# Performance work log

Measured on AMD Instinct MI355X. Metric: run time of the kernel, lower is better.

The kernel has to match this reference:

```python
import jax, jax.numpy as jnp
import numpy as np

DICT_SIZE = 16384
D_MODEL = 1024
TOP_K = 8
B, T = 2, 2048


def setup_inputs() -> dict:
    key = jax.random.key(0)
    k1, k2, k3 = jax.random.split(key, 3)
    x = jax.random.normal(k1, (B, T, D_MODEL), dtype=jnp.float32)
    # nn.Linear weight, scaled small like the torch init style
    W_enc = jax.random.normal(k2, (DICT_SIZE, D_MODEL), dtype=jnp.float32) * 0.02
    # unified dictionary: randn * 0.02 per UnifiedDictionaryCore
    W_dict = jax.random.normal(k3, (DICT_SIZE, D_MODEL), dtype=jnp.float32) * 0.02
    return {"x": x, "W_enc": W_enc, "W_dict": W_dict}


def reference(x, W_enc, W_dict):
    # encoder: Linear(d_model -> dict_size), no bias
    coeffs = jnp.einsum("btd,md->btm", x, W_enc)  # [B,T,dict_size]
    topk_vals, topk_idx = jax.lax.top_k(coeffs, TOP_K)  # [B,T,K]
    # scatter-into-zeros then dense matmul == weighted sum of gathered dict rows
    # (top-k indices are unique per token, so the math is identical)
    rows = W_dict[topk_idx]  # [B,T,K,d_model]
    offset = jnp.einsum("btk,btkd->btd", topk_vals, rows)
    # sparse_coeffs.abs().mean() over the full dense [B,T,dict_size] tensor;
    # only the top-k entries are nonzero
    sparsity_loss = jnp.sum(jnp.abs(topk_vals)) / (coeffs.size)
    return offset, sparsity_loss
```

## Files before the change

kernel.cpp:

```cpp
#include <hip/hip_runtime.h>
#include <float.h>
#include <stdint.h>

constexpr int D_MODEL = 1024;
constexpr int DICT    = 16384;
constexpr int TOPK    = 8;
constexpr int NCAND   = 16;
constexpr int NTOK    = 4096;
constexpr int NTILE   = 128;
constexpr long long COEFF_COUNT = (long long)NTOK * DICT;

typedef __attribute__((ext_vector_type(8))) __bf16 bf16x8;
typedef __attribute__((ext_vector_type(4))) float  floatx4;

__device__ __forceinline__ unsigned short f2bf(float f) {
    unsigned int u = __float_as_uint(f);
    u = u + 0x7fffu + ((u >> 16) & 1u);
    return (unsigned short)(u >> 16);
}

__device__ __forceinline__ void async16(void* lds, const void* g) {
    __builtin_amdgcn_global_load_lds(
        (__attribute__((address_space(1))) void*)g,
        (__attribute__((address_space(3))) void*)lds, 16, 0, 0);
}

__global__ __launch_bounds__(256) void ssod_cvt2(const float4* __restrict__ xs, ushort4* __restrict__ xd, int nx4,
                                                 const float4* __restrict__ ws, ushort4* __restrict__ wd, int nw4) {
    const int i = blockIdx.x * 256 + threadIdx.x;
    if (i < nx4) {
        const float4 v = xs[i];
        ushort4 o; o.x = f2bf(v.x); o.y = f2bf(v.y); o.z = f2bf(v.z); o.w = f2bf(v.w);
        xd[i] = o;
    } else {
        const int j = i - nx4;
        if (j < nw4) {
            const float4 v = ws[j];
            ushort4 o; o.x = f2bf(v.x); o.y = f2bf(v.y); o.z = f2bf(v.z); o.w = f2bf(v.w);
            wd[j] = o;
        }
    }
}

__global__ __launch_bounds__(256) void ssod_gemm_bf16(const unsigned short* __restrict__ A,
                                                      const unsigned short* __restrict__ B,
                                                      unsigned short* __restrict__ C,
                                                      unsigned short* __restrict__ tmax) {
    __shared__ unsigned short As[128 * 32];
    __shared__ unsigned short Bs[128 * 32];
    __shared__ unsigned int rmax[128];

    const int tid  = threadIdx.x;
    const int wave = tid >> 6;
    const int lane = tid & 63;
    const int bn   = blockIdx.x;
    const int bm   = blockIdx.y;
    const int wm   = wave >> 1;
    const int wn   = wave & 1;

    const unsigned short* Abase = A + (size_t)bm * 128 * D_MODEL;
    const unsigned short* Bbase = B + (size_t)bn * 128 * D_MODEL;

    floatx4 acc[4][4];
    #pragma unroll
    for (int i = 0; i < 4; ++i)
        #pragma unroll
        for (int j = 0; j < 4; ++j) acc[i][j] = floatx4{0.f, 0.f, 0.f, 0.f};

    const int c0 = wave * 64 + lane;
    const int c1 = c0 + 256;

    const int fr = lane & 15;
    const int kg = lane >> 4;

    for (int k0 = 0; k0 < D_MODEL; k0 += 32) {
        async16(&As[c0 * 8], Abase + (size_t)(c0 >> 2) * D_MODEL + k0 + (c0 & 3) * 8);
        async16(&As[c1 * 8], Abase + (size_t)(c1 >> 2) * D_MODEL + k0 + (c1 & 3) * 8);
        async16(&Bs[c0 * 8], Bbase + (size_t)(c0 >> 2) * D_MODEL + k0 + (c0 & 3) * 8);
        async16(&Bs[c1 * 8], Bbase + (size_t)(c1 >> 2) * D_MODEL + k0 + (c1 & 3) * 8);
        __syncthreads();

        bf16x8 af[4], bfr[4];
        #pragma unroll
        for (int f = 0; f < 4; ++f) {
            af[f]  = *(const bf16x8*)&As[(wm * 64 + f * 16 + fr) * 32 + kg * 8];
            bfr[f] = *(const bf16x8*)&Bs[(wn * 64 + f * 16 + fr) * 32 + kg * 8];
        }
        #pragma unroll
        for (int i = 0; i < 4; ++i)
            #pragma unroll
            for (int j = 0; j < 4; ++j)
                acc[i][j] = __builtin_amdgcn_mfma_f32_16x16x32_bf16(af[i], bfr[j], acc[i][j], 0, 0, 0);
        __syncthreads();
    }

    if (tid < 128) rmax[tid] = 0;

    const int col = lane & 15;
    const int rq  = lane >> 4;
    unsigned int rowm[4][4];
    #pragma unroll
    for (int i = 0; i < 4; ++i)
        #pragma unroll
        for (int r = 0; r < 4; ++r) rowm[i][r] = 0;

    #pragma unroll
    for (int i = 0; i < 4; ++i) {
        const int row = bm * 128 + wm * 64 + i * 16 + rq * 4;
        #pragma unroll
        for (int j = 0; j < 4; ++j) {
            const int ccol = bn * 128 + wn * 64 + j * 16 + col;
            unsigned short* cp = C + (size_t)row * DICT + ccol;
            #pragma unroll
            for (int r = 0; r < 4; ++r) {
                const unsigned short bf = f2bf(acc[i][j][r]);
                cp[(size_t)r * DICT] = bf;
                rowm[i][r] = max(rowm[i][r], (unsigned int)(bf ^ 0x8000u));
            }
        }
    }
    __syncthreads();

    #pragma unroll
    for (int i = 0; i < 4; ++i)
        #pragma unroll
        for (int r = 0; r < 4; ++r) {
            unsigned int m = rowm[i][r];
            m = max(m, (unsigned int)__shfl_xor((int)m, 1, 64));
            m = max(m, (unsigned int)__shfl_xor((int)m, 2, 64));
            m = max(m, (unsigned int)__shfl_xor((int)m, 4, 64));
            m = max(m, (unsigned int)__shfl_xor((int)m, 8, 64));
            if ((lane & 15) == 0)
                atomicMax(&rmax[wm * 64 + i * 16 + rq * 4 + r], m);
        }
    __syncthreads();

    if (tid < 128)
        tmax[(size_t)(bm * 128 + tid) * NTILE + bn] = (unsigned short)rmax[tid];
}

__device__ __forceinline__ bool tk_better(float v1, int i1, float v2, int i2) {
    return (v1 > v2) || (v1 == v2 && i1 < i2);
}

__global__ __launch_bounds__(256) void ssod_select_refine(const unsigned short* __restrict__ coeffs,
                                                          const unsigned short* __restrict__ tmax,
                                                          const float* __restrict__ x,
                                                          const float* __restrict__ Wenc,
                                                          const float* __restrict__ Wdict,
                                                          float* __restrict__ outp,
                                                          float* __restrict__ tsum,
                                                          int tokBase) {
    const int tl   = blockIdx.x;
    const int t    = tokBase + tl;
    const int tid  = threadIdx.x;
    const int lane = tid & 63;
    const int wave = tid >> 6;

    __shared__ unsigned int keys[128];
    __shared__ int   tlist[64];
    __shared__ int   ncnt, kcnt;
    __shared__ unsigned int sTau;
    __shared__ float xs[D_MODEL];
    __shared__ int   cidx[NCAND];
    __shared__ float cval[NCAND];
    __shared__ float sval[TOPK];
    __shared__ int   sidx[TOPK];

    ((float4*)xs)[tid] = ((const float4*)(x + (size_t)t * D_MODEL))[tid];
    if (tid == 0) { ncnt = 0; kcnt = 0; }
    __syncthreads();

    const unsigned short* tmrow = tmax + (size_t)t * NTILE;
    if (wave == 0) {
        const unsigned int u = ((const unsigned int*)tmrow)[lane];
        unsigned int v0 = u & 0xFFFFu, v1 = u >> 16;
        for (int k = 2; k <= 128; k <<= 1) {
            for (int j = k >> 1; j >= 1; j >>= 1) {
                if (j == 64) {
                    const unsigned int a = max(v0, v1), b = min(v0, v1);
                    v0 = a; v1 = b;
                } else {
                    const unsigned int p0 = __shfl_xor(v0, j, 64);
                    const unsigned int p1 = __shfl_xor(v1, j, 64);
                    const bool tm0 = ((lane & j) == 0) ^ ((( lane      ) & k) != 0);
                    const bool tm1 = ((lane & j) == 0) ^ (((lane + 64) & k) != 0);
                    v0 = tm0 ? max(v0, p0) : min(v0, p0);
                    v1 = tm1 ? max(v1, p1) : min(v1, p1);
                }
            }
        }
        if (lane == 15) sTau = v0;
    }
    __syncthreads();
    const unsigned int tau = sTau;

    if (tid < NTILE) {
        if ((unsigned int)tmrow[tid] >= tau) {
            const int p = atomicAdd(&ncnt, 1);
            if (p < 64) tlist[p] = tid;
        }
    }
    __syncthreads();
    const int nq = min(ncnt, 64);

    const uint4* row4 = (const uint4*)(coeffs + (size_t)tl * DICT);
    for (int j = tid; j < nq * 16; j += 256) {
        const int tile = tlist[j >> 4];
        const int sub  = j & 15;
        const uint4 p = row4[tile * 16 + sub];
        unsigned int w[4] = {p.x ^ 0x80008000u, p.y ^ 0x80008000u,
                             p.z ^ 0x80008000u, p.w ^ 0x80008000u};
        const int base = tile * 128 + sub * 8;
        #pragma unroll
        for (int h = 0; h < 4; ++h) {
            const unsigned int lo = w[h] & 0xFFFFu, hi = w[h] >> 16;
            if (lo >= tau) {
                const int q = atomicAdd(&kcnt, 1);
                if (q < 128) keys[q] = (lo << 16) | (unsigned)(16383 - (base + h * 2));
            }
            if (hi >= tau) {
                const int q = atomicAdd(&kcnt, 1);
                if (q < 128) keys[q] = (hi << 16) | (unsigned)(16383 - (base + h * 2 + 1));
            }
        }
    }
    __syncthreads();
    const int m = min(kcnt, 128);
    for (int i = m + tid; i < 128; i += 256) keys[i] = 0;
    __syncthreads();

    if (wave == 0) {
        unsigned int v0 = keys[lane], v1 = keys[lane + 64];
        for (int k = 2; k <= 128; k <<= 1) {
            for (int j = k >> 1; j >= 1; j >>= 1) {
                if (j == 64) {
                    const unsigned int a = max(v0, v1), b = min(v0, v1);
                    v0 = a; v1 = b;
                } else {
                    const unsigned int p0 = __shfl_xor(v0, j, 64);
                    const unsigned int p1 = __shfl_xor(v1, j, 64);
                    const bool tm0 = ((lane & j) == 0) ^ ((( lane      ) & k) != 0);
                    const bool tm1 = ((lane & j) == 0) ^ (((lane + 64) & k) != 0);
                    v0 = tm0 ? max(v0, p0) : min(v0, p0);
                    v1 = tm1 ? max(v1, p1) : min(v1, p1);
                }
            }
        }
        if (lane < NCAND) cidx[lane] = 16383 - (int)(v0 & 0xFFFFu);
    }
    __syncthreads();

    const float4* xs4 = (const float4*)xs;
    float4 xv[4];
    #pragma unroll
    for (int q = 0; q < 4; ++q) xv[q] = xs4[q * 64 + lane];

    float4 wv[4][4];
    #pragma unroll
    for (int s = 0; s < 4; ++s) {
        const float4* wr4 = (const float4*)(Wenc + (size_t)cidx[s * 4 + wave] * D_MODEL);
        #pragma unroll
        for (int q = 0; q < 4; ++q) wv[s][q] = wr4[q * 64 + lane];
    }
    #pragma unroll
    for (int s = 0; s < 4; ++s) {
        float sum = 0.f;
        #pragma unroll
        for (int q = 0; q < 4; ++q)
            sum += xv[q].x * wv[s][q].x + xv[q].y * wv[s][q].y +
                   xv[q].z * wv[s][q].z + xv[q].w * wv[s][q].w;
        #pragma unroll
        for (int off = 32; off > 0; off >>= 1) sum += __shfl_down(sum, off, 64);
        if (lane == 0) cval[s * 4 + wave] = sum;
    }
    __syncthreads();

    if (tid < NCAND) {
        const float v = cval[tid];
        const int  ix = cidx[tid];
        int rank = 0;
        #pragma unroll
        for (int j = 0; j < NCAND; ++j)
            rank += (j != tid) && tk_better(cval[j], cidx[j], v, ix);
        if (rank < TOPK) { sval[rank] = v; sidx[rank] = ix; }
    }
    __syncthreads();
    if (tid == 0) {
        float s = 0.f;
        #pragma unroll
        for (int k = 0; k < TOPK; ++k) s += fabsf(sval[k]);
        tsum[t] = s;
    }

    const int dd = tid * 4;
    float4 a = make_float4(0.f, 0.f, 0.f, 0.f);
    #pragma unroll
    for (int k = 0; k < TOPK; ++k) {
        const float4 r = *(const float4*)(Wdict + (size_t)sidx[k] * D_MODEL + dd);
        const float s = sval[k];
        a.x += s * r.x; a.y += s * r.y; a.z += s * r.z; a.w += s * r.w;
    }
    *(float4*)(outp + (size_t)t * D_MODEL + dd) = a;
}

__global__ __launch_bounds__(256) void ssod_loss(const float* __restrict__ tsum,
                                                 float* __restrict__ out) {
    float s = 0.f;
    for (int i = threadIdx.x; i < NTOK; i += 256) s += tsum[i];
    #pragma unroll
    for (int off = 32; off > 0; off >>= 1) s += __shfl_down(s, off, 64);
    __shared__ float wsum[4];
    if ((threadIdx.x & 63) == 0) wsum[threadIdx.x >> 6] = s;
    __syncthreads();
    if (threadIdx.x == 0) {
        const float tot = wsum[0] + wsum[1] + wsum[2] + wsum[3];
        out[(size_t)NTOK * D_MODEL] = tot / (float)COEFF_COUNT;
    }
}

extern "C" void kernel_launch(void* const* d_in, const int* in_sizes, int n_in,
                              void* d_out, int out_size, void* d_ws, size_t ws_size,
                              hipStream_t stream) {
    const float* x     = (const float*)d_in[0];
    const float* Wenc  = (const float*)d_in[1];
    const float* Wdict = (const float*)d_in[2];
    float* out = (float*)d_out;

    char* ws = (char*)d_ws;
    size_t off = 0;
    unsigned short* xbf  = (unsigned short*)(ws + off); off += (size_t)NTOK * D_MODEL * 2;
    unsigned short* wbf  = (unsigned short*)(ws + off); off += (size_t)DICT * D_MODEL * 2;
    unsigned short* tmax = (unsigned short*)(ws + off); off += (size_t)NTOK * NTILE * 2;
    float* tsum = (float*)(ws + off);                   off += (size_t)NTOK * 4;
    unsigned short* coeffs = (unsigned short*)(ws + off);

    const size_t remain = (ws_size > off) ? (ws_size - off) : 0;
    int chunk = 512;
    if (remain >= (size_t)4096 * DICT * 2) chunk = 4096;
    else if (remain >= (size_t)2048 * DICT * 2) chunk = 2048;
    else if (remain >= (size_t)1024 * DICT * 2) chunk = 1024;

    const int nx4 = NTOK * D_MODEL / 4;
    const int nw4 = DICT * D_MODEL / 4;
    ssod_cvt2<<<(nx4 + nw4 + 255) / 256, 256, 0, stream>>>(
        (const float4*)x, (ushort4*)xbf, nx4, (const float4*)Wenc, (ushort4*)wbf, nw4);

    for (int tokBase = 0; tokBase < NTOK; tokBase += chunk) {
        dim3 g(DICT / 128, chunk / 128);
        ssod_gemm_bf16<<<g, 256, 0, stream>>>(xbf + (size_t)tokBase * D_MODEL, wbf, coeffs,
                                              tmax + (size_t)tokBase * NTILE);
        ssod_select_refine<<<chunk, 256, 0, stream>>>(coeffs, tmax, x, Wenc, Wdict, out, tsum, tokBase);
    }
    ssod_loss<<<1, 256, 0, stream>>>(tsum, out);
}
```

Before: 393.6 us.

## Rewrite encoder GEMM with 256x256 tiles, 4-stage async pipeline and swizzled LDS

Replaces the 128x128 single-buffered bf16 GEMM with a 512-thread, 256x256-tile kernel. It uses a 4-deep ring of LDS buffers filled by async global-to-LDS loads, XOR-swizzled LDS layout to avoid bank conflicts, interleaved barriers with s_setprio around MFMA bursts, and an XCD-aware block remapping. This targets load latency exposure and low arithmetic intensity in the old GEMM, at the cost of higher register and LDS pressure. The kernel now hardcodes 32 k-tiles and requires the chunk size to be a multiple of 256.

```diff
diff --git a/kernel.cpp b/kernel.cpp
--- a/kernel.cpp
+++ b/kernel.cpp
@@ -42,102 +42,165 @@
     }
 }
 
-__global__ __launch_bounds__(256) void ssod_gemm_bf16(const unsigned short* __restrict__ A,
-                                                      const unsigned short* __restrict__ B,
-                                                      unsigned short* __restrict__ C,
-                                                      unsigned short* __restrict__ tmax) {
-    __shared__ unsigned short As[128 * 32];
-    __shared__ unsigned short Bs[128 * 32];
-    __shared__ unsigned int rmax[128];
+constexpr size_t R1OFF = (size_t)128 * (D_MODEL * 2);
+
+#define STAGE_A(buf_, t_) do {                                               \
+    const char* s_ = pA + (size_t)(t_) * 64;                                 \
+    char* d_ = (char*)&As[(buf_)][0] + wave * 1024;                          \
+    async16(d_, s_); async16(d_ + 8192, s_ + R1OFF);                         \
+} while (0)
+
+#define STAGE_B(buf_, t_) do {                                               \
+    const char* s_ = pB + (size_t)(t_) * 64;                                 \
+    char* d_ = (char*)&Bs[(buf_)][0] + wave * 1024;                          \
+    async16(d_, s_); async16(d_ + 8192, s_ + R1OFF);                         \
+} while (0)
+
+#define MFMA4(a_, r_)                                                                        \
+    acc[r_][0] = __builtin_amdgcn_mfma_f32_16x16x32_bf16(a_, bq0, acc[r_][0], 0, 0, 0);      \
+    acc[r_][1] = __builtin_amdgcn_mfma_f32_16x16x32_bf16(a_, bq1, acc[r_][1], 0, 0, 0);      \
+    acc[r_][2] = __builtin_amdgcn_mfma_f32_16x16x32_bf16(a_, bq2, acc[r_][2], 0, 0, 0);      \
+    acc[r_][3] = __builtin_amdgcn_mfma_f32_16x16x32_bf16(a_, bq3, acc[r_][3], 0, 0, 0);
+
+#define TILE_BODY(T_, DOSTAGE_)                                              \
+  {                                                                          \
+    const int buf_ = (T_) & 3;                                               \
+    const char* ab_ = (const char*)As + buf_ * 16384 + aob;                  \
+    const char* bb_ = (const char*)Bs + buf_ * 16384 + bob;                  \
+    bf16x8 af0 = *(const bf16x8*)(ab_);                                      \
+    bf16x8 af1 = *(const bf16x8*)(ab_ + 1024);                               \
+    bf16x8 af2 = *(const bf16x8*)(ab_ + 2048);                               \
+    bf16x8 af3 = *(const bf16x8*)(ab_ + 3072);                               \
+    bf16x8 bq0 = *(const bf16x8*)(bb_);                                      \
+    bf16x8 bq1 = *(const bf16x8*)(bb_ + 1024);                               \
+    bf16x8 bq2 = *(const bf16x8*)(bb_ + 2048);                               \
+    bf16x8 bq3 = *(const bf16x8*)(bb_ + 3072);                               \
+    if (DOSTAGE_) { STAGE_A(((T_) + 3) & 3, (T_) + 3); }                     \
+    __builtin_amdgcn_s_barrier();                                            \
+    asm volatile("s_waitcnt lgkmcnt(0)" ::: "memory");                       \
+    __builtin_amdgcn_s_setprio(1);                                           \
+    MFMA4(af0, 0); MFMA4(af1, 1); MFMA4(af2, 2); MFMA4(af3, 3);              \
+    __builtin_amdgcn_s_setprio(0);                                           \
+    __builtin_amdgcn_s_barrier();                                            \
+    bf16x8 ag0 = *(const bf16x8*)(ab_ + 4096);                               \
+    bf16x8 ag1 = *(const bf16x8*)(ab_ + 5120);                               \
+    bf16x8 ag2 = *(const bf16x8*)(ab_ + 6144);                               \
+    bf16x8 ag3 = *(const bf16x8*)(ab_ + 7168);                               \
+    if (DOSTAGE_) { STAGE_B(((T_) + 3) & 3, (T_) + 3); }                     \
+    __builtin_amdgcn_s_barrier();                                            \
+    asm volatile("s_waitcnt lgkmcnt(0)" ::: "memory");                       \
+    __builtin_amdgcn_s_setprio(1);                                           \
+    MFMA4(ag0, 4); MFMA4(ag1, 5); MFMA4(ag2, 6); MFMA4(ag3, 7);              \
+    __builtin_amdgcn_s_setprio(0);                                           \
+  }
+
+#define TILE_CLOSE(VMI)                                                      \
+    asm volatile("s_waitcnt vmcnt(" #VMI ")" ::: "memory");                  \
+    __builtin_amdgcn_s_barrier();
+
+__global__ __launch_bounds__(512, 2) void ssod_gemm_bf16(const unsigned short* __restrict__ A,
+                                                         const unsigned short* __restrict__ B,
+                                                         unsigned short* __restrict__ C,
+                                                         unsigned short* __restrict__ tmax,
+                                                         int mtiles) {
+    __shared__ __align__(16) unsigned short As[4][8192];
+    __shared__ __align__(16) unsigned short Bs[4][8192];
 
     const int tid  = threadIdx.x;
     const int wave = tid >> 6;
     const int lane = tid & 63;
-    const int bn   = blockIdx.x;
-    const int bm   = blockIdx.y;
-    const int wm   = wave >> 1;
-    const int wn   = wave & 1;
-
-    const unsigned short* Abase = A + (size_t)bm * 128 * D_MODEL;
-    const unsigned short* Bbase = B + (size_t)bn * 128 * D_MODEL;
-
-    floatx4 acc[4][4];
-    #pragma unroll
-    for (int i = 0; i < 4; ++i)
-        #pragma unroll
-        for (int j = 0; j < 4; ++j) acc[i][j] = floatx4{0.f, 0.f, 0.f, 0.f};
-
-    const int c0 = wave * 64 + lane;
-    const int c1 = c0 + 256;
-
+
+    const int nwg = mtiles * 64;
+    const int cpx = nwg >> 3;
+    const int bid = blockIdx.x;
+    const int vid = (bid & 7) * cpx + (bid >> 3);
+    const int bn  = vid & 63;
+    const int bm  = vid >> 6;
+
+    const int wm = wave >> 2;
+    const int wn = wave & 3;
     const int fr = lane & 15;
     const int kg = lane >> 4;
 
-    for (int k0 = 0; k0 < D_MODEL; k0 += 32) {
-        async16(&As[c0 * 8], Abase + (size_t)(c0 >> 2) * D_MODEL + k0 + (c0 & 3) * 8);
-        async16(&As[c1 * 8], Abase + (size_t)(c1 >> 2) * D_MODEL + k0 + (c1 & 3) * 8);
-        async16(&Bs[c0 * 8], Bbase + (size_t)(c0 >> 2) * D_MODEL + k0 + (c0 & 3) * 8);
-        async16(&Bs[c1 * 8], Bbase + (size_t)(c1 >> 2) * D_MODEL + k0 + (c1 & 3) * 8);
-        __syncthreads();
-
-        bf16x8 af[4], bfr[4];
-        #pragma unroll
-        for (int f = 0; f < 4; ++f) {
-            af[f]  = *(const bf16x8*)&As[(wm * 64 + f * 16 + fr) * 32 + kg * 8];
-            bfr[f] = *(const bf16x8*)&Bs[(wn * 64 + f * 16 + fr) * 32 + kg * 8];
-        }
-        #pragma unroll
-        for (int i = 0; i < 4; ++i)
-            #pragma unroll
-            for (int j = 0; j < 4; ++j)
-                acc[i][j] = __builtin_amdgcn_mfma_f32_16x16x32_bf16(af[i], bfr[j], acc[i][j], 0, 0, 0);
-        __syncthreads();
-    }
-
-    if (tid < 128) rmax[tid] = 0;
-
-    const int col = lane & 15;
-    const int rq  = lane >> 4;
-    unsigned int rowm[4][4];
-    #pragma unroll
-    for (int i = 0; i < 4; ++i)
-        #pragma unroll
-        for (int r = 0; r < 4; ++r) rowm[i][r] = 0;
-
-    #pragma unroll
-    for (int i = 0; i < 4; ++i) {
-        const int row = bm * 128 + wm * 64 + i * 16 + rq * 4;
-        #pragma unroll
-        for (int j = 0; j < 4; ++j) {
-            const int ccol = bn * 128 + wn * 64 + j * 16 + col;
-            unsigned short* cp = C + (size_t)row * DICT + ccol;
+    const int sR   = tid >> 3;
+    const int sinp = ((tid & 7) * 16) ^ ((sR & 7) << 4);
+    const int smr  = 2 * sR + (sinp >> 6);
+    const int skb  = sinp & 63;
+    const char* pA = (const char*)(A + (size_t)bm * 256 * D_MODEL) + (size_t)smr * (D_MODEL * 2) + skb;
+    const char* pB = (const char*)(B + (size_t)bn * 256 * D_MODEL) + (size_t)smr * (D_MODEL * 2) + skb;
+
+    const int swz = ((((fr & 1) << 6) | (kg << 4)) ^ (((fr >> 1) & 7) << 4));
+    const int aob = (wm * 64 + (fr >> 1)) * 128 + swz;
+    const int bob = (wn * 32 + (fr >> 1)) * 128 + swz;
+
+    floatx4 acc[8][4];
+    #pragma unroll
+    for (int i = 0; i < 8; ++i)
+        #pragma unroll
+        for (int j = 0; j < 4; ++j) acc[i][j] = floatx4{0.f, 0.f, 0.f, 0.f};
+
+    STAGE_A(0, 0); STAGE_B(0, 0);
+    STAGE_A(1, 1); STAGE_B(1, 1);
+    STAGE_A(2, 2); STAGE_B(2, 2);
+    TILE_CLOSE(8)
+
+    #pragma unroll 1
+    for (int T = 0; T < 29; ++T) {
+        TILE_BODY(T, true)
+        TILE_CLOSE(8)
+    }
+    TILE_BODY(29, false)
+    TILE_CLOSE(4)
+    TILE_BODY(30, false)
+    TILE_CLOSE(0)
+    TILE_BODY(31, false)
+
+    __syncthreads();
+    unsigned int* rmax = (unsigned int*)&As[0][0];
+    rmax[tid] = 0;
+    __syncthreads();
+
+    const int col  = lane & 15;
+    const int rq   = lane >> 4;
+    const int half = wn >> 1;
+    const size_t colbase = (size_t)bn * 256 + wn * 64 + col;
+
+    #pragma unroll
+    for (int mf = 0; mf < 8; ++mf) {
+        const int rowl = wm * 128 + mf * 16 + rq * 4;
+        unsigned int rm[4] = {0, 0, 0, 0};
+        #pragma unroll
+        for (int nf = 0; nf < 4; ++nf) {
+            unsigned short* cp = C + (size_t)(bm * 256 + rowl) * DICT + colbase + nf * 16;
             #pragma unroll
             for (int r = 0; r < 4; ++r) {
-                const unsigned short bf = f2bf(acc[i][j][r]);
-                cp[(size_t)r * DICT] = bf;
-                rowm[i][r] = max(rowm[i][r], (unsigned int)(bf ^ 0x8000u));
+                const unsigned short bfv = f2bf(acc[mf][nf][r]);
+                cp[(size_t)r * DICT] = bfv;
+                rm[r] = max(rm[r], (unsigned int)(bfv ^ 0x8000u));
             }
         }
-    }
-    __syncthreads();
-
-    #pragma unroll
-    for (int i = 0; i < 4; ++i)
         #pragma unroll
         for (int r = 0; r < 4; ++r) {
-            unsigned int m = rowm[i][r];
+            unsigned int m = rm[r];
             m = max(m, (unsigned int)__shfl_xor((int)m, 1, 64));
             m = max(m, (unsigned int)__shfl_xor((int)m, 2, 64));
             m = max(m, (unsigned int)__shfl_xor((int)m, 4, 64));
             m = max(m, (unsigned int)__shfl_xor((int)m, 8, 64));
-            if ((lane & 15) == 0)
-                atomicMax(&rmax[wm * 64 + i * 16 + rq * 4 + r], m);
-        }
-    __syncthreads();
-
-    if (tid < 128)
-        tmax[(size_t)(bm * 128 + tid) * NTILE + bn] = (unsigned short)rmax[tid];
-}
+            if (col == 0) atomicMax(&rmax[(rowl + r) * 2 + half], m);
+        }
+    }
+    __syncthreads();
+    {
+        const int row = tid >> 1;
+        tmax[(size_t)(bm * 256 + row) * NTILE + bn * 2 + (tid & 1)] = (unsigned short)rmax[tid];
+    }
+}
+
+#undef TILE_BODY
+#undef TILE_CLOSE
+#undef MFMA4
+#undef STAGE_A
+#undef STAGE_B
 
 __device__ __forceinline__ bool tk_better(float v1, int i1, float v2, int i2) {
     return (v1 > v2) || (v1 == v2 && i1 < i2);
@@ -347,9 +410,9 @@
         (const float4*)x, (ushort4*)xbf, nx4, (const float4*)Wenc, (ushort4*)wbf, nw4);
 
     for (int tokBase = 0; tokBase < NTOK; tokBase += chunk) {
-        dim3 g(DICT / 128, chunk / 128);
-        ssod_gemm_bf16<<<g, 256, 0, stream>>>(xbf + (size_t)tokBase * D_MODEL, wbf, coeffs,
-                                              tmax + (size_t)tokBase * NTILE);
+        const int mtiles = chunk / 256;
+        ssod_gemm_bf16<<<mtiles * 64, 512, 0, stream>>>(xbf + (size_t)tokBase * D_MODEL, wbf, coeffs,
+                                                        tmax + (size_t)tokBase * NTILE, mtiles);
         ssod_select_refine<<<chunk, 256, 0, stream>>>(coeffs, tmax, x, Wenc, Wdict, out, tsum, tokBase);
     }
     ssod_loss<<<1, 256, 0, stream>>>(tsum, out);
```

Measured after the change: 397.6 us. Within noise of the previous version (+1.0%).
